# Optimization experiments

Measured on AMD Instinct MI355X. Metric: run time of the kernel, lower is better.

The kernel has to match this reference:

```python
import jax, jax.numpy as jnp
import numpy as np

B, N, F, K = 512, 512, 512, 10
D = F // 2

def setup_inputs() -> dict:
    key = jax.random.key(0)
    k1, k2, k3 = jax.random.split(key, 3)
    ins_emb = jax.random.normal(k1, (B, N, F), dtype=jnp.float32)
    attn = jax.random.uniform(k2, (B, N, 1), dtype=jnp.float32)
    # xavier_uniform for a (D, D) linear weight
    limit = float(np.sqrt(6.0 / (D + D)))
    W = jax.random.uniform(k3, (D, D), dtype=jnp.float32, minval=-limit, maxval=limit)
    return {"ins_emb": ins_emb, "attn": attn, "W": W}

def reference(ins_emb, attn, W):
    d = ins_emb.shape[-1] // 2
    drug = ins_emb[:, :, :d]          # [B, N, d]
    dis = ins_emb[:, :, d:]           # [B, N, d]
    # torch Linear: drug @ W^T, then per-instance dot with dis -> scalar
    proj = jnp.einsum('bnd,ed->bne', drug, W)          # [B, N, d]
    pred = jnp.sum(proj * dis, axis=-1, keepdims=True) # [B, N, 1]
    attn_pred = attn * pred                            # [B, N, 1]
    topk_vals, _ = jax.lax.top_k(attn_pred[:, :, 0], K)  # [B, K]
    return jnp.mean(topk_vals, axis=1, keepdims=True)    # [B, 1]
```

## Files before the change

### kernel.cpp

```cpp
#include <hip/hip_runtime.h>
#include <hip/hip_bf16.h>
#include <cstdint>

#define BB 512
#define NN 512
#define FF 512
#define DD 256
#define KTOP 10
#define BN (BB*NN)
#define BM 64
#define NTILES (BN/BM)
#define LDAP 264

typedef __attribute__((ext_vector_type(8))) short bf16x8;
typedef __attribute__((ext_vector_type(4))) short s16x4;
typedef __attribute__((ext_vector_type(4))) float f32x4;

__device__ __forceinline__ ushort f2bf(float x){
  uint32_t u = __float_as_uint(x);
  uint32_t r = (u + 0x7FFFu + ((u >> 16) & 1u)) >> 16;
  return (ushort)r;
}
__device__ __forceinline__ float bf2f(ushort b){
  return __uint_as_float(((uint32_t)b) << 16);
}

__global__ void wconv(const float* __restrict__ W, ushort* __restrict__ Wbf){
  int i = (blockIdx.x*256 + threadIdx.x)*4;
  float4 v = *reinterpret_cast<const float4*>(W + i);
  s16x4 o;
  o[0] = (short)f2bf(v.x); o[1] = (short)f2bf(v.y);
  o[2] = (short)f2bf(v.z); o[3] = (short)f2bf(v.w);
  *reinterpret_cast<s16x4*>(Wbf + i) = o;
}

__global__ __launch_bounds__(256, 2)
void score_kernel(const float* __restrict__ emb, const float* __restrict__ attn,
                  const ushort* __restrict__ Wbf, float* __restrict__ scores){
  __shared__ ushort Al[BM*LDAP];
  __shared__ ushort Sl[BM*LDAP];
  __shared__ float red[4][BM];

  const int tid  = threadIdx.x;
  const int w    = tid >> 6;
  const int lane = tid & 63;
  const int g    = lane >> 4;
  const int c    = lane & 15;

  bf16x8 Wf[4][8];
#pragma unroll
  for (int eb = 0; eb < 4; ++eb)
#pragma unroll
    for (int kb = 0; kb < 8; ++kb){
      int e = w*64 + eb*16 + c;
      int k = kb*32 + g*8;
      Wf[eb][kb] = *reinterpret_cast<const bf16x8*>(Wbf + e*DD + k);
    }

  const int ch = tid & 63;
  const int rsub = tid >> 6;

  for (int tile = blockIdx.x; tile < NTILES; tile += gridDim.x){
    const float* base = emb + (size_t)tile * BM * FF;

#pragma unroll
    for (int it = 0; it < 16; ++it){
      int row = it*4 + rsub;
      const float* src = base + row*FF + ch*8;
      float4 v0 = *reinterpret_cast<const float4*>(src);
      float4 v1 = *reinterpret_cast<const float4*>(src + 4);
      bf16x8 p;
      p[0]=(short)f2bf(v0.x); p[1]=(short)f2bf(v0.y); p[2]=(short)f2bf(v0.z); p[3]=(short)f2bf(v0.w);
      p[4]=(short)f2bf(v1.x); p[5]=(short)f2bf(v1.y); p[6]=(short)f2bf(v1.z); p[7]=(short)f2bf(v1.w);
      ushort* dst = (ch < 32) ? (Al + row*LDAP + ch*8)
                              : (Sl + row*LDAP + (ch-32)*8);
      *reinterpret_cast<bf16x8*>(dst) = p;
    }
    __syncthreads();

    for (int mb = 0; mb < 4; ++mb){
      const int m0 = mb*16;
      bf16x8 af[8];
#pragma unroll
      for (int kb = 0; kb < 8; ++kb)
        af[kb] = *reinterpret_cast<const bf16x8*>(Al + (m0 + c)*LDAP + kb*32 + g*8);
      float rs0=0.f, rs1=0.f, rs2=0.f, rs3=0.f;
#pragma unroll
      for (int eb = 0; eb < 4; ++eb){
        f32x4 acc = {0.f, 0.f, 0.f, 0.f};
#pragma unroll
        for (int kb = 0; kb < 8; ++kb)
          acc = __builtin_amdgcn_mfma_f32_16x16x32_bf16(af[kb], Wf[eb][kb], acc, 0, 0, 0);
        const int e_loc = w*64 + eb*16 + c;
        rs0 += acc[0] * bf2f(Sl[(m0 + g*4 + 0)*LDAP + e_loc]);
        rs1 += acc[1] * bf2f(Sl[(m0 + g*4 + 1)*LDAP + e_loc]);
        rs2 += acc[2] * bf2f(Sl[(m0 + g*4 + 2)*LDAP + e_loc]);
        rs3 += acc[3] * bf2f(Sl[(m0 + g*4 + 3)*LDAP + e_loc]);
      }
      float r0=rs0, r1=rs1, r2=rs2, r3=rs3;
      r0 += __shfl_xor(r0,1); r0 += __shfl_xor(r0,2); r0 += __shfl_xor(r0,4); r0 += __shfl_xor(r0,8);
      r1 += __shfl_xor(r1,1); r1 += __shfl_xor(r1,2); r1 += __shfl_xor(r1,4); r1 += __shfl_xor(r1,8);
      r2 += __shfl_xor(r2,1); r2 += __shfl_xor(r2,2); r2 += __shfl_xor(r2,4); r2 += __shfl_xor(r2,8);
      r3 += __shfl_xor(r3,1); r3 += __shfl_xor(r3,2); r3 += __shfl_xor(r3,4); r3 += __shfl_xor(r3,8);
      if (c == 0){
        red[w][m0 + g*4 + 0] = r0;
        red[w][m0 + g*4 + 1] = r1;
        red[w][m0 + g*4 + 2] = r2;
        red[w][m0 + g*4 + 3] = r3;
      }
    }
    __syncthreads();
    if (tid < BM){
      int row = tile*BM + tid;
      float s = red[0][tid] + red[1][tid] + red[2][tid] + red[3][tid];
      scores[row] = attn[row] * s;
    }
    __syncthreads();
  }
}

__global__ void topk_kernel(const float* __restrict__ scores, float* __restrict__ out){
  const int b = blockIdx.x;
  const int lane = threadIdx.x;
  float v0,v1,v2,v3,v4,v5,v6,v7;
  const float* s = scores + b*NN;
  v0=s[lane]; v1=s[64+lane]; v2=s[128+lane]; v3=s[192+lane];
  v4=s[256+lane]; v5=s[320+lane]; v6=s[384+lane]; v7=s[448+lane];
  float total = 0.f;
  for (int it = 0; it < KTOP; ++it){
    float m = v0; int mj = 0;
    if (v1>m){m=v1;mj=1;} if (v2>m){m=v2;mj=2;} if (v3>m){m=v3;mj=3;}
    if (v4>m){m=v4;mj=4;} if (v5>m){m=v5;mj=5;} if (v6>m){m=v6;mj=6;}
    if (v7>m){m=v7;mj=7;}
    float bm = m; int bl = lane;
#pragma unroll
    for (int off = 32; off; off >>= 1){
      float om = __shfl_xor(bm, off);
      int   ol = __shfl_xor(bl, off);
      if (om > bm || (om == bm && ol < bl)){ bm = om; bl = ol; }
    }
    total += bm;
    if (lane == bl){
      if (mj==0) v0=-3.0e38f; else if (mj==1) v1=-3.0e38f;
      else if (mj==2) v2=-3.0e38f; else if (mj==3) v3=-3.0e38f;
      else if (mj==4) v4=-3.0e38f; else if (mj==5) v5=-3.0e38f;
      else if (mj==6) v6=-3.0e38f; else v7=-3.0e38f;
    }
  }
  if (lane == 0) out[b] = total * (1.0f / KTOP);
}

extern "C" void kernel_launch(void* const* d_in, const int* in_sizes, int n_in,
                              void* d_out, int out_size, void* d_ws, size_t ws_size,
                              hipStream_t stream){
  const float* emb  = (const float*)d_in[0];
  const float* attn = (const float*)d_in[1];
  const float* W    = (const float*)d_in[2];
  float* out = (float*)d_out;

  ushort* Wbf   = (ushort*)d_ws;
  float*  scores = (float*)((char*)d_ws + DD*DD*sizeof(ushort));

  wconv<<<64, 256, 0, stream>>>(W, Wbf);
  score_kernel<<<512, 256, 0, stream>>>(emb, attn, Wbf, scores);
  topk_kernel<<<BB, 64, 0, stream>>>(scores, out);
}
```

Baseline: 122.5 us.

## Double-buffer drug tile in LDS with register prefetch; read disease half directly

Result: slower. 156.2 us (+27.5%).

```diff
diff --git a/kernel.cpp b/kernel.cpp
--- a/kernel.cpp
+++ b/kernel.cpp
@@ -8,8 +8,10 @@
 #define DD 256
 #define KTOP 10
 #define BN (BB*NN)
-#define BM 64
+#define BM 32
 #define NTILES (BN/BM)
+#define GRID 512
+#define TPB (NTILES/GRID)
 #define LDAP 264
 
 typedef __attribute__((ext_vector_type(8))) short bf16x8;
@@ -17,12 +19,9 @@
 typedef __attribute__((ext_vector_type(4))) float f32x4;
 
 __device__ __forceinline__ ushort f2bf(float x){
-  uint32_t u = __float_as_uint(x);
-  uint32_t r = (u + 0x7FFFu + ((u >> 16) & 1u)) >> 16;
-  return (ushort)r;
-}
-__device__ __forceinline__ float bf2f(ushort b){
-  return __uint_as_float(((uint32_t)b) << 16);
+  union { __hip_bfloat16 h; ushort u; } cv;
+  cv.h = __float2bfloat16(x);
+  return cv.u;
 }
 
 __global__ void wconv(const float* __restrict__ W, ushort* __restrict__ Wbf){
@@ -37,8 +36,7 @@
 __global__ __launch_bounds__(256, 2)
 void score_kernel(const float* __restrict__ emb, const float* __restrict__ attn,
                   const ushort* __restrict__ Wbf, float* __restrict__ scores){
-  __shared__ ushort Al[BM*LDAP];
-  __shared__ ushort Sl[BM*LDAP];
+  __shared__ ushort Abuf[2][BM*LDAP];
   __shared__ float red[4][BM];
 
   const int tid  = threadIdx.x;
@@ -57,33 +55,61 @@
       Wf[eb][kb] = *reinterpret_cast<const bf16x8*>(Wbf + e*DD + k);
     }
 
-  const int ch = tid & 63;
-  const int rsub = tid >> 6;
+  const int ch   = tid & 31;
+  const int rsub = tid >> 5;
+  const int tile0 = blockIdx.x * TPB;
 
-  for (int tile = blockIdx.x; tile < NTILES; tile += gridDim.x){
-    const float* base = emb + (size_t)tile * BM * FF;
+  float4 pf[8];
+
+#define PF_LOAD(TILE) do {                                                   \
+    const float* base_ = emb + (size_t)(TILE)*BM*FF;                         \
+    _Pragma("unroll")                                                        \
+    for (int it = 0; it < 4; ++it){                                          \
+      const float* src_ = base_ + (it*8 + rsub)*FF + ch*8;                   \
+      pf[it*2]   = *reinterpret_cast<const float4*>(src_);                   \
+      pf[it*2+1] = *reinterpret_cast<const float4*>(src_ + 4);               \
+    }                                                                        \
+  } while(0)
+
+#define LDS_WRITE(BUFI) do {                                                 \
+    _Pragma("unroll")                                                        \
+    for (int it = 0; it < 4; ++it){                                          \
+      float4 a_ = pf[it*2], b_ = pf[it*2+1];                                 \
+      bf16x8 p_;                                                             \
+      p_[0]=(short)f2bf(a_.x); p_[1]=(short)f2bf(a_.y);                      \
+      p_[2]=(short)f2bf(a_.z); p_[3]=(short)f2bf(a_.w);                      \
+      p_[4]=(short)f2bf(b_.x); p_[5]=(short)f2bf(b_.y);                      \
+      p_[6]=(short)f2bf(b_.z); p_[7]=(short)f2bf(b_.w);                      \
+      *reinterpret_cast<bf16x8*>(&Abuf[BUFI][(it*8 + rsub)*LDAP + ch*8]) = p_;\
+    }                                                                        \
+  } while(0)
+
+  PF_LOAD(tile0);
+  LDS_WRITE(0);
+  __syncthreads();
+
+  int cur = 0;
+  for (int t = 0; t < TPB; ++t){
+    const int tile = tile0 + t;
+    if (t + 1 < TPB) PF_LOAD(tile + 1);
+
+    const float* disp = emb + (size_t)tile*BM*FF + DD;
 
 #pragma unroll
-    for (int it = 0; it < 16; ++it){
-      int row = it*4 + rsub;
-      const float* src = base + row*FF + ch*8;
-      float4 v0 = *reinterpret_cast<const float4*>(src);
-      float4 v1 = *reinterpret_cast<const float4*>(src + 4);
-      bf16x8 p;
-      p[0]=(short)f2bf(v0.x); p[1]=(short)f2bf(v0.y); p[2]=(short)f2bf(v0.z); p[3]=(short)f2bf(v0.w);
-      p[4]=(short)f2bf(v1.x); p[5]=(short)f2bf(v1.y); p[6]=(short)f2bf(v1.z); p[7]=(short)f2bf(v1.w);
-      ushort* dst = (ch < 32) ? (Al + row*LDAP + ch*8)
-                              : (Sl + row*LDAP + (ch-32)*8);
-      *reinterpret_cast<bf16x8*>(dst) = p;
-    }
-    __syncthreads();
-
-    for (int mb = 0; mb < 4; ++mb){
+    for (int mb = 0; mb < 2; ++mb){
       const int m0 = mb*16;
       bf16x8 af[8];
 #pragma unroll
       for (int kb = 0; kb < 8; ++kb)
-        af[kb] = *reinterpret_cast<const bf16x8*>(Al + (m0 + c)*LDAP + kb*32 + g*8);
+        af[kb] = *reinterpret_cast<const bf16x8*>(&Abuf[cur][(m0 + c)*LDAP + kb*32 + g*8]);
+
+      float dv[16];
+#pragma unroll
+      for (int j = 0; j < 4; ++j)
+#pragma unroll
+        for (int eb = 0; eb < 4; ++eb)
+          dv[j*4+eb] = disp[(m0 + g*4 + j)*FF + w*64 + eb*16 + c];
+
       float rs0=0.f, rs1=0.f, rs2=0.f, rs3=0.f;
 #pragma unroll
       for (int eb = 0; eb < 4; ++eb){
@@ -91,32 +117,33 @@
 #pragma unroll
         for (int kb = 0; kb < 8; ++kb)
           acc = __builtin_amdgcn_mfma_f32_16x16x32_bf16(af[kb], Wf[eb][kb], acc, 0, 0, 0);
-        const int e_loc = w*64 + eb*16 + c;
-        rs0 += acc[0] * bf2f(Sl[(m0 + g*4 + 0)*LDAP + e_loc]);
-        rs1 += acc[1] * bf2f(Sl[(m0 + g*4 + 1)*LDAP + e_loc]);
-        rs2 += acc[2] * bf2f(Sl[(m0 + g*4 + 2)*LDAP + e_loc]);
-        rs3 += acc[3] * bf2f(Sl[(m0 + g*4 + 3)*LDAP + e_loc]);
+        rs0 += acc[0] * dv[0*4+eb];
+        rs1 += acc[1] * dv[1*4+eb];
+        rs2 += acc[2] * dv[2*4+eb];
+        rs3 += acc[3] * dv[3*4+eb];
       }
-      float r0=rs0, r1=rs1, r2=rs2, r3=rs3;
-      r0 += __shfl_xor(r0,1); r0 += __shfl_xor(r0,2); r0 += __shfl_xor(r0,4); r0 += __shfl_xor(r0,8);
-      r1 += __shfl_xor(r1,1); r1 += __shfl_xor(r1,2); r1 += __shfl_xor(r1,4); r1 += __shfl_xor(r1,8);
-      r2 += __shfl_xor(r2,1); r2 += __shfl_xor(r2,2); r2 += __shfl_xor(r2,4); r2 += __shfl_xor(r2,8);
-      r3 += __shfl_xor(r3,1); r3 += __shfl_xor(r3,2); r3 += __shfl_xor(r3,4); r3 += __shfl_xor(r3,8);
+      rs0 += __shfl_xor(rs0,1); rs0 += __shfl_xor(rs0,2); rs0 += __shfl_xor(rs0,4); rs0 += __shfl_xor(rs0,8);
+      rs1 += __shfl_xor(rs1,1); rs1 += __shfl_xor(rs1,2); rs1 += __shfl_xor(rs1,4); rs1 += __shfl_xor(rs1,8);
+      rs2 += __shfl_xor(rs2,1); rs2 += __shfl_xor(rs2,2); rs2 += __shfl_xor(rs2,4); rs2 += __shfl_xor(rs2,8);
+      rs3 += __shfl_xor(rs3,1); rs3 += __shfl_xor(rs3,2); rs3 += __shfl_xor(rs3,4); rs3 += __shfl_xor(rs3,8);
       if (c == 0){
-        red[w][m0 + g*4 + 0] = r0;
-        red[w][m0 + g*4 + 1] = r1;
-        red[w][m0 + g*4 + 2] = r2;
-        red[w][m0 + g*4 + 3] = r3;
+        red[w][m0 + g*4 + 0] = rs0;
+        red[w][m0 + g*4 + 1] = rs1;
+        red[w][m0 + g*4 + 2] = rs2;
+        red[w][m0 + g*4 + 3] = rs3;
       }
     }
     __syncthreads();
     if (tid < BM){
       int row = tile*BM + tid;
-      float s = red[0][tid] + red[1][tid] + red[2][tid] + red[3][tid];
-      scores[row] = attn[row] * s;
+      scores[row] = attn[row] * (red[0][tid] + red[1][tid] + red[2][tid] + red[3][tid]);
     }
+    if (t + 1 < TPB) LDS_WRITE(cur ^ 1);
     __syncthreads();
+    cur ^= 1;
   }
+#undef PF_LOAD
+#undef LDS_WRITE
 }
 
 __global__ void topk_kernel(const float* __restrict__ scores, float* __restrict__ out){
@@ -158,10 +185,10 @@
   const float* W    = (const float*)d_in[2];
   float* out = (float*)d_out;
 
-  ushort* Wbf   = (ushort*)d_ws;
+  ushort* Wbf    = (ushort*)d_ws;
   float*  scores = (float*)((char*)d_ws + DD*DD*sizeof(ushort));
 
   wconv<<<64, 256, 0, stream>>>(W, Wbf);
-  score_kernel<<<512, 256, 0, stream>>>(emb, attn, Wbf, scores);
+  score_kernel<<<GRID, 256, 0, stream>>>(emb, attn, Wbf, scores);
   topk_kernel<<<BB, 64, 0, stream>>>(scores, out);
 }
```
